# Kernel optimization log

Hardware: AMD Instinct MI355X
Metric: run time of the kernel (lower is better)

The kernel has to match this reference:

```python
import jax, jax.numpy as jnp
import numpy as np
from jax import lax

VOCAB = 50000; EMB = 128; HID = 256; NL = 9; B = 128; T = 512; H = HID // 2; PAD = 0


def setup_inputs() -> dict:
    key = jax.random.key(0)
    ks = jax.random.split(key, 16)
    p = lambda k, s: jax.random.normal(k, s, jnp.float32) * 0.05
    return {
        "chars": jax.random.randint(ks[0], (B, T), 1, VOCAB),  # in [1, VOCAB) so mask fully on
        "labels": jax.random.randint(ks[1], (B, T), 0, NL),
        "emb": p(ks[2], (VOCAB, EMB)),
        "W_ih_f": p(ks[3], (4 * H, EMB)), "W_hh_f": p(ks[4], (4 * H, H)),
        "b_ih_f": p(ks[5], (4 * H,)), "b_hh_f": p(ks[6], (4 * H,)),
        "W_ih_b": p(ks[7], (4 * H, EMB)), "W_hh_b": p(ks[8], (4 * H, H)),
        "b_ih_b": p(ks[9], (4 * H,)), "b_hh_b": p(ks[10], (4 * H,)),
        "W_out": p(ks[11], (NL, HID)), "b_out": p(ks[12], (NL,)),
        "start_trans": p(ks[13], (NL,)), "end_trans": p(ks[14], (NL,)),
        "trans": p(ks[15], (NL, NL)),
    }


def _lstm(x, Wih, Whh, bih, bhh, reverse):
    # x: (B, T, D); PyTorch gate order i, f, g, o
    bsz = x.shape[0]
    h0 = jnp.zeros((bsz, H), x.dtype)
    c0 = jnp.zeros((bsz, H), x.dtype)
    b = bih + bhh

    def step(carry, xt):
        h, c = carry
        g = xt @ Wih.T + h @ Whh.T + b  # (B, 4H)
        i, f, gg, o = jnp.split(g, 4, axis=-1)
        c = jax.nn.sigmoid(f) * c + jax.nn.sigmoid(i) * jnp.tanh(gg)
        h = jax.nn.sigmoid(o) * jnp.tanh(c)
        return (h, c), h

    _, hs = lax.scan(step, (h0, c0), jnp.swapaxes(x, 0, 1), reverse=reverse)
    return jnp.swapaxes(hs, 0, 1)  # (B, T, H)


def _crf_nll(emissions, labels, mask, start, end, trans):
    # torchcrf linear-chain CRF log-likelihood, reduction='sum'
    maskf = mask.astype(emissions.dtype)
    emit = jnp.take_along_axis(emissions, labels[..., None], 2)[..., 0]  # (B, T)
    score = start[labels[:, 0]] + (emit * maskf).sum(1)
    score = score + (trans[labels[:, :-1], labels[:, 1:]] * maskf[:, 1:]).sum(1)
    last_idx = mask.sum(1).astype(jnp.int32) - 1
    last_tags = jnp.take_along_axis(labels, last_idx[:, None], 1)[:, 0]
    score = score + end[last_tags]

    # forward algorithm (log partition) as a scan over time
    alpha0 = start[None, :] + emissions[:, 0]  # (B, L)

    def step(alpha, inp):
        e_t, m_t = inp  # (B, L), (B,)
        nxt = jax.nn.logsumexp(alpha[:, :, None] + trans[None, :, :], axis=1) + e_t
        return jnp.where(m_t[:, None], nxt, alpha), None

    alpha, _ = lax.scan(step, alpha0,
                        (jnp.swapaxes(emissions, 0, 1)[1:], jnp.swapaxes(mask, 0, 1)[1:]))
    logZ = jax.nn.logsumexp(alpha + end[None, :], axis=-1)
    return -(score - logZ).sum()


def reference(chars, labels, emb, W_ih_f, W_hh_f, b_ih_f, b_hh_f,
              W_ih_b, W_hh_b, b_ih_b, b_hh_b, W_out, b_out,
              start_trans, end_trans, trans):
    x = emb[chars]  # (B, T, EMB)
    hf = _lstm(x, W_ih_f, W_hh_f, b_ih_f, b_hh_f, False)
    hb = _lstm(x, W_ih_b, W_hh_b, b_ih_b, b_hh_b, True)
    h = jnp.concatenate([hf, hb], axis=-1)  # (B, T, HID)
    emissions = h @ W_out.T + b_out  # dropout is identity in eval mode
    mask = chars != PAD
    return _crf_nll(emissions, labels, mask, start_trans, end_trans, trans)
```

## Files before the change

kernel.cpp:

```cpp
#include <hip/hip_runtime.h>

#define B_   128
#define T_   512
#define EMB_ 128
#define H_   128
#define G4_  512
#define NG_  1024
#define NL_  9
#define MT_  65536

typedef __attribute__((ext_vector_type(8))) short short8v;
typedef __attribute__((ext_vector_type(4))) float float4v;

__device__ inline unsigned short f2bf(float f){
  unsigned u = __float_as_uint(f);
  u += 0x7FFFu + ((u >> 16) & 1u);
  return (unsigned short)(u >> 16);
}
__device__ inline float bf2f(unsigned short s){
  return __uint_as_float(((unsigned)s) << 16);
}
__device__ inline float sigm(float x){ return 1.f / (1.f + __expf(-x)); }
__device__ inline float tanh_(float x){ return 2.f / (1.f + __expf(-2.f * x)) - 1.f; }

__global__ void k0_prep(const float* __restrict__ Wf, const float* __restrict__ Wb,
                        const float* __restrict__ bihf, const float* __restrict__ bhhf,
                        const float* __restrict__ bihb, const float* __restrict__ bhhb,
                        unsigned short* __restrict__ Wcat, float* __restrict__ biasc){
  int n = blockIdx.x;
  int k = threadIdx.x;
  const float* src = (n < G4_) ? (Wf + n * EMB_) : (Wb + (n - G4_) * EMB_);
  Wcat[n * EMB_ + k] = f2bf(src[k]);
  if (k == 0)
    biasc[n] = (n < G4_) ? (bihf[n] + bhhf[n]) : (bihb[n - G4_] + bhhb[n - G4_]);
}

__global__ void k1_embed(const int* __restrict__ chars, const float* __restrict__ emb,
                         unsigned short* __restrict__ x){
  int i = blockIdx.x * blockDim.x + threadIdx.x;
  int m = i >> 5, q = i & 31;
  int c = chars[m];
  const float4* e4 = (const float4*)(emb + (long)c * EMB_);
  float4 v = e4[q];
  ushort4 o;
  o.x = f2bf(v.x); o.y = f2bf(v.y); o.z = f2bf(v.z); o.w = f2bf(v.w);
  *(ushort4*)(x + (long)m * EMB_ + q * 4) = o;
}

__global__ __launch_bounds__(256) void k2_gemm(const unsigned short* __restrict__ x,
                                               const unsigned short* __restrict__ Wcat,
                                               const float* __restrict__ biasc,
                                               unsigned short* __restrict__ G){
  int w = threadIdx.x >> 6, lane = threadIdx.x & 63;
  int r = lane & 15, kb = (lane >> 4) * 8;
  long arow = (long)(blockIdx.x * 64 + w * 16 + r);
  short8v a[4];
  #pragma unroll
  for (int kf = 0; kf < 4; kf++)
    a[kf] = *(const short8v*)(x + arow * EMB_ + kf * 32 + kb);
  int ncol0 = blockIdx.y * 128;
  float4v acc[8];
  #pragma unroll
  for (int nf = 0; nf < 8; nf++){
    float4v z = {0.f, 0.f, 0.f, 0.f};
    acc[nf] = z;
    int wrow = ncol0 + nf * 16 + r;
    #pragma unroll
    for (int kf = 0; kf < 4; kf++){
      short8v bfrag = *(const short8v*)(Wcat + (long)wrow * EMB_ + kf * 32 + kb);
      acc[nf] = __builtin_amdgcn_mfma_f32_16x16x32_bf16(a[kf], bfrag, acc[nf], 0, 0, 0);
    }
  }
  int crow0 = blockIdx.x * 64 + w * 16 + (lane >> 4) * 4;
  #pragma unroll
  for (int nf = 0; nf < 8; nf++){
    int col = ncol0 + nf * 16 + r;
    float bia = biasc[col];
    #pragma unroll
    for (int reg = 0; reg < 4; reg++)
      G[(long)(crow0 + reg) * NG_ + col] = f2bf(acc[nf][reg] + bia);
  }
}

__global__ __launch_bounds__(512, 2) void k3_scan(const unsigned short* __restrict__ G,
                                                  const float* __restrict__ Whhf,
                                                  const float* __restrict__ Whhb,
                                                  unsigned short* __restrict__ hs){
  int dir = blockIdx.x >> 7;
  int b   = blockIdx.x & 127;
  int j   = threadIdx.x;
  const float* Whh = dir ? Whhb : Whhf;
  float4 w[32];
  #pragma unroll
  for (int q = 0; q < 32; q++) w[q] = *(const float4*)(Whh + (long)j * H_ + q * 4);
  __shared__ __align__(16) float h[H_];
  __shared__ float g[G4_];
  if (j < H_) h[j] = 0.f;
  float c = 0.f;
  __syncthreads();
  const float4* h4 = (const float4*)h;
  for (int s = 0; s < T_; s++){
    int t = dir ? (T_ - 1 - s) : s;
    long m = (long)b * T_ + t;
    float gv = bf2f(G[m * NG_ + dir * G4_ + j]);
    float a0 = 0.f, a1 = 0.f, a2 = 0.f, a3 = 0.f;
    #pragma unroll
    for (int q = 0; q < 32; q++){
      float4 hv = h4[q];
      a0 = fmaf(w[q].x, hv.x, a0);
      a1 = fmaf(w[q].y, hv.y, a1);
      a2 = fmaf(w[q].z, hv.z, a2);
      a3 = fmaf(w[q].w, hv.w, a3);
    }
    g[j] = gv + (a0 + a1) + (a2 + a3);
    __syncthreads();
    if (j < H_){
      float iv = sigm(g[j]);
      float fv = sigm(g[j + 128]);
      float gg = tanh_(g[j + 256]);
      float ov = sigm(g[j + 384]);
      c = fv * c + iv * gg;
      float hv = ov * tanh_(c);
      h[j] = hv;
      hs[((long)dir * MT_ + m) * H_ + j] = f2bf(hv);
    }
    __syncthreads();
  }
}

#define HSTR 264
__global__ __launch_bounds__(512) void k4_emis(const unsigned short* __restrict__ hs,
                                               const float* __restrict__ Wout,
                                               const float* __restrict__ bout,
                                               float* __restrict__ em){
  __shared__ float hcat[64 * HSTR];
  __shared__ float wo[NL_ * 256];
  int tid = threadIdx.x;
  int m0 = blockIdx.x * 64;
  const unsigned short* hf = hs;
  const unsigned short* hb = hs + (long)MT_ * H_;
  #pragma unroll
  for (int it = 0; it < 8; it++){
    int flat = it * 2048 + tid * 4;
    int r = flat >> 8, u = flat & 255;
    const unsigned short* src = (u < 128) ? (hf + (long)(m0 + r) * H_ + u)
                                          : (hb + (long)(m0 + r) * H_ + (u - 128));
    ushort4 v = *(const ushort4*)src;
    hcat[r * HSTR + u]     = bf2f(v.x);
    hcat[r * HSTR + u + 1] = bf2f(v.y);
    hcat[r * HSTR + u + 2] = bf2f(v.z);
    hcat[r * HSTR + u + 3] = bf2f(v.w);
  }
  for (int f = tid; f < NL_ * 256; f += 512) wo[f] = Wout[f];
  __syncthreads();
  #pragma unroll
  for (int half = 0; half < 2; half++){
    int idx = half * 512 + tid;
    if (idx < 64 * NL_){
      int r = idx / NL_, l = idx % NL_;
      float acc = bout[l];
      #pragma unroll 8
      for (int u = 0; u < 256; u++)
        acc = fmaf(hcat[r * HSTR + u], wo[l * 256 + u], acc);
      em[(long)(m0 + r) * NL_ + l] = acc;
    }
  }
}

__global__ void k5_crf(const float* __restrict__ em, const int* __restrict__ chars,
                       const int* __restrict__ labels, const float* __restrict__ startv,
                       const float* __restrict__ endv, const float* __restrict__ trans,
                       float* __restrict__ partial){
  int b = blockIdx.x, lane = threadIdx.x;
  const int* lab = labels + b * T_;
  const int* ch  = chars + b * T_;
  const float* e = em + (long)b * T_ * NL_;
  float sc = 0.f; int cnt = 0;
  for (int t = lane; t < T_; t += 64){
    int m = (ch[t] != 0);
    cnt += m;
    if (m){
      sc += e[t * NL_ + lab[t]];
      if (t > 0) sc += trans[lab[t - 1] * NL_ + lab[t]];
    }
  }
  #pragma unroll
  for (int off = 32; off; off >>= 1){
    sc  += __shfl_down(sc, off);
    cnt += __shfl_down(cnt, off);
  }
  sc  = __shfl(sc, 0);
  cnt = __shfl(cnt, 0);
  if (cnt < 1) cnt = 1;
  int jl = (lane < NL_) ? lane : 0;
  float tcol[NL_];
  #pragma unroll
  for (int i = 0; i < NL_; i++) tcol[i] = trans[i * NL_ + jl];
  float alpha = (lane < NL_) ? (startv[jl] + e[jl]) : -1e30f;
  for (int t = 1; t < T_; t++){
    int m = (ch[t] != 0);
    float ev = (lane < NL_) ? e[t * NL_ + jl] : 0.f;
    float vv[NL_]; float mx = -1e30f;
    #pragma unroll
    for (int i = 0; i < NL_; i++){
      vv[i] = __shfl(alpha, i) + tcol[i];
      mx = fmaxf(mx, vv[i]);
    }
    float ssum = 0.f;
    #pragma unroll
    for (int i = 0; i < NL_; i++) ssum += __expf(vv[i] - mx);
    float nxt = mx + __logf(ssum) + ev;
    if (m && lane < NL_) alpha = nxt;
  }
  float av = (lane < NL_) ? (alpha + endv[jl]) : -1e30f;
  float mx = av;
  #pragma unroll
  for (int off = 8; off; off >>= 1) mx = fmaxf(mx, __shfl_down(mx, off));
  mx = __shfl(mx, 0);
  float ex = (lane < NL_) ? __expf(av - mx) : 0.f;
  #pragma unroll
  for (int off = 8; off; off >>= 1) ex += __shfl_down(ex, off);
  if (lane == 0){
    float logZ = mx + __logf(ex);
    float score = sc + startv[lab[0]] + endv[lab[cnt - 1]];
    partial[b] = logZ - score;
  }
}

__global__ void k6_reduce(const float* __restrict__ partial, float* __restrict__ out){
  int lane = threadIdx.x;
  float v = partial[lane];
  #pragma unroll
  for (int off = 32; off; off >>= 1) v += __shfl_down(v, off);
  __shared__ float tmp[2];
  if ((lane & 63) == 0) tmp[lane >> 6] = v;
  __syncthreads();
  if (lane == 0) out[0] = tmp[0] + tmp[1];
}

extern "C" void kernel_launch(void* const* d_in, const int* in_sizes, int n_in,
                              void* d_out, int out_size, void* d_ws, size_t ws_size,
                              hipStream_t stream){
  const int*   chars  = (const int*)d_in[0];
  const int*   labels = (const int*)d_in[1];
  const float* emb    = (const float*)d_in[2];
  const float* Wihf   = (const float*)d_in[3];
  const float* Whhf   = (const float*)d_in[4];
  const float* bihf   = (const float*)d_in[5];
  const float* bhhf   = (const float*)d_in[6];
  const float* Wihb   = (const float*)d_in[7];
  const float* Whhb   = (const float*)d_in[8];
  const float* bihb   = (const float*)d_in[9];
  const float* bhhb   = (const float*)d_in[10];
  const float* Wout   = (const float*)d_in[11];
  const float* bout   = (const float*)d_in[12];
  const float* startv = (const float*)d_in[13];
  const float* endv   = (const float*)d_in[14];
  const float* trans  = (const float*)d_in[15];

  char* ws = (char*)d_ws;
  unsigned short* x     = (unsigned short*)(ws);
  unsigned short* Wcat  = (unsigned short*)(ws + 16777216);
  float*          biasc = (float*)         (ws + 17039360);
  unsigned short* G     = (unsigned short*)(ws + 17043456);
  unsigned short* hs    = (unsigned short*)(ws + 151261184);
  float*          em    = (float*)         (ws + 184815616);
  float*          part  = (float*)         (ws + 187174912);

  hipLaunchKernelGGL(k0_prep,  dim3(1024),     dim3(128), 0, stream,
                     Wihf, Wihb, bihf, bhhf, bihb, bhhb, Wcat, biasc);
  hipLaunchKernelGGL(k1_embed, dim3(8192),     dim3(256), 0, stream, chars, emb, x);
  hipLaunchKernelGGL(k2_gemm,  dim3(1024, 8),  dim3(256), 0, stream, x, Wcat, biasc, G);
  hipLaunchKernelGGL(k3_scan,  dim3(256),      dim3(512), 0, stream, G, Whhf, Whhb, hs);
  hipLaunchKernelGGL(k4_emis,  dim3(1024),     dim3(512), 0, stream, hs, Wout, bout, em);
  hipLaunchKernelGGL(k5_crf,   dim3(128),      dim3(64),  0, stream,
                     em, chars, labels, startv, endv, trans, part);
  hipLaunchKernelGGL(k6_reduce, dim3(1),       dim3(128), 0, stream, part, (float*)d_out);
}
```

Before: 1.087 ms.

## Fuse input projection into MFMA-based LSTM scan over 16-row batch tiles

Drops the separate input-projection GEMM and its large bf16 gate buffer. A fused kernel computes both h@Whh and x@Wih with bf16 MFMA inside the recurrence, processing 16 batch rows per block and keeping the weights in registers. Hidden states go through double-buffered LDS and are written out every 8 steps in batches. The CRF kernel also prefetches the next step's emission and mask. In exchange, only 16 blocks run the scan, and the recurrent weights and h are now held in bf16, which lowers precision.

```diff
diff --git a/kernel.cpp b/kernel.cpp
--- a/kernel.cpp
+++ b/kernel.cpp
@@ -4,8 +4,6 @@
 #define T_   512
 #define EMB_ 128
 #define H_   128
-#define G4_  512
-#define NG_  1024
 #define NL_  9
 #define MT_  65536
 
@@ -23,16 +21,24 @@
 __device__ inline float sigm(float x){ return 1.f / (1.f + __expf(-x)); }
 __device__ inline float tanh_(float x){ return 2.f / (1.f + __expf(-2.f * x)) - 1.f; }
 
-__global__ void k0_prep(const float* __restrict__ Wf, const float* __restrict__ Wb,
+__global__ void k0_prep(const float* __restrict__ Wihf, const float* __restrict__ Whhf,
                         const float* __restrict__ bihf, const float* __restrict__ bhhf,
+                        const float* __restrict__ Wihb, const float* __restrict__ Whhb,
                         const float* __restrict__ bihb, const float* __restrict__ bhhb,
-                        unsigned short* __restrict__ Wcat, float* __restrict__ biasc){
-  int n = blockIdx.x;
-  int k = threadIdx.x;
-  const float* src = (n < G4_) ? (Wf + n * EMB_) : (Wb + (n - G4_) * EMB_);
-  Wcat[n * EMB_ + k] = f2bf(src[k]);
-  if (k == 0)
-    biasc[n] = (n < G4_) ? (bihf[n] + bhhf[n]) : (bihb[n - G4_] + bhhb[n - G4_]);
+                        unsigned short* __restrict__ Wall, float* __restrict__ biasc){
+  int blk = blockIdx.x;
+  int dir = blk >> 9;
+  int n   = blk & 511;
+  int k   = threadIdx.x;
+  const float* Wih = dir ? Wihb : Wihf;
+  const float* Whh = dir ? Whhb : Whhf;
+  float v = (k < 128) ? Whh[n * H_ + k] : Wih[n * EMB_ + (k - 128)];
+  Wall[((long)(dir * 512 + n)) * 256 + k] = f2bf(v);
+  if (k == 0){
+    const float* bi = dir ? bihb : bihf;
+    const float* bh = dir ? bhhb : bhhf;
+    biasc[dir * 512 + n] = bi[n] + bh[n];
+  }
 }
 
 __global__ void k1_embed(const int* __restrict__ chars, const float* __restrict__ emb,
@@ -47,84 +53,108 @@
   *(ushort4*)(x + (long)m * EMB_ + q * 4) = o;
 }
 
-__global__ __launch_bounds__(256) void k2_gemm(const unsigned short* __restrict__ x,
-                                               const unsigned short* __restrict__ Wcat,
-                                               const float* __restrict__ biasc,
-                                               unsigned short* __restrict__ G){
-  int w = threadIdx.x >> 6, lane = threadIdx.x & 63;
-  int r = lane & 15, kb = (lane >> 4) * 8;
-  long arow = (long)(blockIdx.x * 64 + w * 16 + r);
-  short8v a[4];
-  #pragma unroll
-  for (int kf = 0; kf < 4; kf++)
-    a[kf] = *(const short8v*)(x + arow * EMB_ + kf * 32 + kb);
-  int ncol0 = blockIdx.y * 128;
-  float4v acc[8];
-  #pragma unroll
-  for (int nf = 0; nf < 8; nf++){
-    float4v z = {0.f, 0.f, 0.f, 0.f};
-    acc[nf] = z;
-    int wrow = ncol0 + nf * 16 + r;
+__global__ __launch_bounds__(512, 2) void k3_fused(
+    const unsigned short* __restrict__ x,
+    const unsigned short* __restrict__ Wall,
+    const float* __restrict__ biasc,
+    unsigned short* __restrict__ hs)
+{
+  const int blk = blockIdx.x;
+  const int dir = blk >> 3;
+  const int b0  = (blk & 7) * 16;
+  const int tid = threadIdx.x;
+  const int w   = tid >> 6;
+  const int l   = tid & 63;
+  const int r   = l & 15;
+  const int q   = l >> 4;
+  const int jcol = w * 16 + r;
+
+  __shared__ unsigned short hA[2][2048];
+  __shared__ unsigned short hbuf[8][16][128];
+
+  short8v Bf[4][8];
+  #pragma unroll
+  for (int g = 0; g < 4; g++){
+    const unsigned short* wp = Wall + ((long)(dir * 512 + g * 128 + jcol)) * 256 + q * 8;
+    #pragma unroll
+    for (int kf = 0; kf < 8; kf++)
+      Bf[g][kf] = *(const short8v*)(wp + kf * 32);
+  }
+  float bias[4];
+  #pragma unroll
+  for (int g = 0; g < 4; g++) bias[g] = biasc[dir * 512 + g * 128 + jcol];
+
+  for (int i = tid; i < 2048; i += 512) hA[0][i] = 0;
+
+  float cc[4] = {0.f, 0.f, 0.f, 0.f};
+  const int hAoff = (jcol >> 5) * 512 + ((jcol & 31) >> 3) * 128 + (jcol & 7);
+
+  short8v xnxt[4];
+  {
+    int t0 = dir ? (T_ - 1) : 0;
+    #pragma unroll
+    for (int kf = 0; kf < 4; kf++)
+      xnxt[kf] = *(const short8v*)(x + ((long)(b0 + r) * T_ + t0) * EMB_ + kf * 32 + q * 8);
+  }
+  __syncthreads();
+
+  for (int s = 0; s < T_; s++){
+    const int p = s & 1;
+    short8v xcur[4];
+    #pragma unroll
+    for (int kf = 0; kf < 4; kf++) xcur[kf] = xnxt[kf];
+    {
+      int sn = (s + 1 < T_) ? s + 1 : s;
+      int tn = dir ? (T_ - 1 - sn) : sn;
+      #pragma unroll
+      for (int kf = 0; kf < 4; kf++)
+        xnxt[kf] = *(const short8v*)(x + ((long)(b0 + r) * T_ + tn) * EMB_ + kf * 32 + q * 8);
+    }
+
+    float4v acc[4];
+    #pragma unroll
+    for (int g = 0; g < 4; g++){ float4v z = {0.f,0.f,0.f,0.f}; acc[g] = z; }
     #pragma unroll
     for (int kf = 0; kf < 4; kf++){
-      short8v bfrag = *(const short8v*)(Wcat + (long)wrow * EMB_ + kf * 32 + kb);
-      acc[nf] = __builtin_amdgcn_mfma_f32_16x16x32_bf16(a[kf], bfrag, acc[nf], 0, 0, 0);
-    }
-  }
-  int crow0 = blockIdx.x * 64 + w * 16 + (lane >> 4) * 4;
-  #pragma unroll
-  for (int nf = 0; nf < 8; nf++){
-    int col = ncol0 + nf * 16 + r;
-    float bia = biasc[col];
-    #pragma unroll
-    for (int reg = 0; reg < 4; reg++)
-      G[(long)(crow0 + reg) * NG_ + col] = f2bf(acc[nf][reg] + bia);
-  }
-}
-
-__global__ __launch_bounds__(512, 2) void k3_scan(const unsigned short* __restrict__ G,
-                                                  const float* __restrict__ Whhf,
-                                                  const float* __restrict__ Whhb,
-                                                  unsigned short* __restrict__ hs){
-  int dir = blockIdx.x >> 7;
-  int b   = blockIdx.x & 127;
-  int j   = threadIdx.x;
-  const float* Whh = dir ? Whhb : Whhf;
-  float4 w[32];
-  #pragma unroll
-  for (int q = 0; q < 32; q++) w[q] = *(const float4*)(Whh + (long)j * H_ + q * 4);
-  __shared__ __align__(16) float h[H_];
-  __shared__ float g[G4_];
-  if (j < H_) h[j] = 0.f;
-  float c = 0.f;
-  __syncthreads();
-  const float4* h4 = (const float4*)h;
-  for (int s = 0; s < T_; s++){
-    int t = dir ? (T_ - 1 - s) : s;
-    long m = (long)b * T_ + t;
-    float gv = bf2f(G[m * NG_ + dir * G4_ + j]);
-    float a0 = 0.f, a1 = 0.f, a2 = 0.f, a3 = 0.f;
-    #pragma unroll
-    for (int q = 0; q < 32; q++){
-      float4 hv = h4[q];
-      a0 = fmaf(w[q].x, hv.x, a0);
-      a1 = fmaf(w[q].y, hv.y, a1);
-      a2 = fmaf(w[q].z, hv.z, a2);
-      a3 = fmaf(w[q].w, hv.w, a3);
-    }
-    g[j] = gv + (a0 + a1) + (a2 + a3);
+      short8v af = *(const short8v*)&hA[p][(kf * 4 + q) * 128 + r * 8];
+      #pragma unroll
+      for (int g = 0; g < 4; g++)
+        acc[g] = __builtin_amdgcn_mfma_f32_16x16x32_bf16(af, Bf[g][kf], acc[g], 0, 0, 0);
+    }
+    #pragma unroll
+    for (int kf = 0; kf < 4; kf++){
+      #pragma unroll
+      for (int g = 0; g < 4; g++)
+        acc[g] = __builtin_amdgcn_mfma_f32_16x16x32_bf16(xcur[kf], Bf[g][kf + 4], acc[g], 0, 0, 0);
+    }
+
+    #pragma unroll
+    for (int reg = 0; reg < 4; reg++){
+      int m = q * 4 + reg;
+      float iv = sigm(acc[0][reg] + bias[0]);
+      float fv = sigm(acc[1][reg] + bias[1]);
+      float gg = tanh_(acc[2][reg] + bias[2]);
+      float ov = sigm(acc[3][reg] + bias[3]);
+      cc[reg] = fv * cc[reg] + iv * gg;
+      float hv = ov * tanh_(cc[reg]);
+      unsigned short hb = f2bf(hv);
+      hA[p ^ 1][hAoff + m * 8] = hb;
+      hbuf[s & 7][m][jcol] = hb;
+    }
     __syncthreads();
-    if (j < H_){
-      float iv = sigm(g[j]);
-      float fv = sigm(g[j + 128]);
-      float gg = tanh_(g[j + 256]);
-      float ov = sigm(g[j + 384]);
-      c = fv * c + iv * gg;
-      float hv = ov * tanh_(c);
-      h[j] = hv;
-      hs[((long)dir * MT_ + m) * H_ + j] = f2bf(hv);
-    }
-    __syncthreads();
+
+    if ((s & 7) == 7){
+      #pragma unroll
+      for (int mr = 0; mr < 4; mr++){
+        int u  = tid + mr * 512;
+        int j8 = u & 15, mm = (u >> 4) & 15, ii = u >> 8;
+        int sg = s - 7 + ii;
+        int tg = dir ? (T_ - 1 - sg) : sg;
+        short8v v = *(const short8v*)&hbuf[ii][mm][j8 * 8];
+        *(short8v*)(hs + ((long)dir * MT_ + (long)(b0 + mm) * T_ + tg) * H_ + j8 * 8) = v;
+      }
+      __syncthreads();
+    }
   }
 }
 
@@ -157,12 +187,12 @@
   for (int half = 0; half < 2; half++){
     int idx = half * 512 + tid;
     if (idx < 64 * NL_){
-      int r = idx / NL_, l = idx % NL_;
-      float acc = bout[l];
+      int r = idx / NL_, lbl = idx % NL_;
+      float acc = bout[lbl];
       #pragma unroll 8
       for (int u = 0; u < 256; u++)
-        acc = fmaf(hcat[r * HSTR + u], wo[l * 256 + u], acc);
-      em[(long)(m0 + r) * NL_ + l] = acc;
+        acc = fmaf(hcat[r * HSTR + u], wo[lbl * 256 + u], acc);
+      em[(long)(m0 + r) * NL_ + lbl] = acc;
     }
   }
 }
@@ -197,9 +227,13 @@
   #pragma unroll
   for (int i = 0; i < NL_; i++) tcol[i] = trans[i * NL_ + jl];
   float alpha = (lane < NL_) ? (startv[jl] + e[jl]) : -1e30f;
+  float evn = (lane < NL_) ? e[NL_ + jl] : 0.f;
+  int   mn  = (ch[1] != 0);
   for (int t = 1; t < T_; t++){
-    int m = (ch[t] != 0);
-    float ev = (lane < NL_) ? e[t * NL_ + jl] : 0.f;
+    float ev = evn; int m = mn;
+    int t2 = (t + 1 < T_) ? t + 1 : t;
+    evn = (lane < NL_) ? e[t2 * NL_ + jl] : 0.f;
+    mn  = (ch[t2] != 0);
     float vv[NL_]; float mx = -1e30f;
     #pragma unroll
     for (int i = 0; i < NL_; i++){
@@ -260,20 +294,18 @@
 
   char* ws = (char*)d_ws;
   unsigned short* x     = (unsigned short*)(ws);
-  unsigned short* Wcat  = (unsigned short*)(ws + 16777216);
-  float*          biasc = (float*)         (ws + 17039360);
-  unsigned short* G     = (unsigned short*)(ws + 17043456);
-  unsigned short* hs    = (unsigned short*)(ws + 151261184);
-  float*          em    = (float*)         (ws + 184815616);
-  float*          part  = (float*)         (ws + 187174912);
-
-  hipLaunchKernelGGL(k0_prep,  dim3(1024),     dim3(128), 0, stream,
-                     Wihf, Wihb, bihf, bhhf, bihb, bhhb, Wcat, biasc);
-  hipLaunchKernelGGL(k1_embed, dim3(8192),     dim3(256), 0, stream, chars, emb, x);
-  hipLaunchKernelGGL(k2_gemm,  dim3(1024, 8),  dim3(256), 0, stream, x, Wcat, biasc, G);
-  hipLaunchKernelGGL(k3_scan,  dim3(256),      dim3(512), 0, stream, G, Whhf, Whhb, hs);
-  hipLaunchKernelGGL(k4_emis,  dim3(1024),     dim3(512), 0, stream, hs, Wout, bout, em);
-  hipLaunchKernelGGL(k5_crf,   dim3(128),      dim3(64),  0, stream,
+  unsigned short* Wall  = (unsigned short*)(ws + 16777216);
+  float*          biasc = (float*)         (ws + 17301504);
+  unsigned short* hs    = (unsigned short*)(ws + 17305600);
+  float*          em    = (float*)         (ws + 50860032);
+  float*          part  = (float*)         (ws + 53219328);
+
+  hipLaunchKernelGGL(k0_prep,  dim3(1024), dim3(256), 0, stream,
+                     Wihf, Whhf, bihf, bhhf, Wihb, Whhb, bihb, bhhb, Wall, biasc);
+  hipLaunchKernelGGL(k1_embed, dim3(8192), dim3(256), 0, stream, chars, emb, x);
+  hipLaunchKernelGGL(k3_fused, dim3(16),   dim3(512), 0, stream, x, Wall, biasc, hs);
+  hipLaunchKernelGGL(k4_emis,  dim3(1024), dim3(512), 0, stream, hs, Wout, bout, em);
+  hipLaunchKernelGGL(k5_crf,   dim3(128),  dim3(64),  0, stream,
                      em, chars, labels, startv, endv, trans, part);
-  hipLaunchKernelGGL(k6_reduce, dim3(1),       dim3(128), 0, stream, part, (float*)d_out);
-}
+  hipLaunchKernelGGL(k6_reduce, dim3(1),   dim3(128), 0, stream, part, (float*)d_out);
+}
```

New measurement: 1.131 ms. 1.04x slower.
